# Performance work log

Measured on AMD Instinct MI355X. Metric: run time of the kernel, lower is better.

## Reference

```python
import jax, jax.numpy as jnp
import numpy as np

B, H, P, D, NF = 16, 16, 128, 128, 12  # patches == head_dim required by lin_qk


def setup_inputs() -> dict:
    key = jax.random.key(0)
    ks = jax.random.split(key, 8)
    return {
        "q": jax.random.normal(ks[0], (B, H, P, D), jnp.float32),
        "k": jax.random.normal(ks[1], (B, H, P, D), jnp.float32),
        "scale": jnp.ones((1,), jnp.float32),  # unused by the original forward
        "grid": jnp.arange(NF, dtype=jnp.float32) + 1.0,
        "base_weight": jax.random.uniform(ks[2], (D, D), jnp.float32),
        "coef_q": jax.random.uniform(ks[3], (D, NF), jnp.float32),
        "coef_k": jax.random.uniform(ks[4], (D, NF), jnp.float32),
        "scale_base": jnp.ones((1, H, P, D), jnp.float32),
        "scale_sp": jnp.ones((1, H, P, D), jnp.float32),
        "w_qk": jax.random.normal(ks[5], (D, D), jnp.float32) / np.float32(np.sqrt(D)),
        "b_qk": jnp.zeros((D,), jnp.float32),
    }


def _branch(x, coef, grid, base_weight, scale_sp, scale_base):
    # base path: SiLU(x) @ W^T  (F.linear semantics)
    base = jax.nn.silu(x) @ base_weight.T
    # KAN sin basis: sin(grid_f * x_d) -> (B,H,P,NF,D); contract coef[d,f]
    s = jnp.sin(grid[:, None] * x[..., None, :])
    f = jnp.einsum('df,bhpfd->bhpd', coef, s)
    return jax.nn.sigmoid(f * scale_sp + base * scale_base)


def reference(q, k, scale, grid, base_weight, coef_q, coef_k, scale_base, scale_sp, w_qk, b_qk):
    # Per-channel sigmoids, then sum over D. The original builds the full
    # (B,H,P,P,D) broadcast tensor sig_q[...,p,None,:] + sig_k[...,None,p',:]
    # and sums over D; that is exactly separable:
    #   sum_d(sig_q[p,d]) + sum_d(sig_k[p',d])
    sq = _branch(q, coef_q, grid, base_weight, scale_sp, scale_base).sum(-1)  # (B,H,P)
    sk = _branch(k, coef_k, grid, base_weight, scale_sp, scale_base).sum(-1)  # (B,H,P)
    f_out = sq[..., :, None] + sk[..., None, :]  # (B,H,P,P)
    f_out = f_out @ w_qk.T + b_qk  # lin_qk: valid because patches == head_dim
    return jax.nn.softmax(f_out, axis=-1)
```

## Files before the change

kernel.cpp:

```cpp
#include <hip/hip_runtime.h>
#include <hip/hip_bf16.h>


typedef float          f32x4 __attribute__((ext_vector_type(4)));
typedef short          s16x8 __attribute__((ext_vector_type(8)));
typedef unsigned short u16x8 __attribute__((ext_vector_type(8)));

static __device__ __forceinline__ unsigned short f2bf(float f) {
    __hip_bfloat16 h = __float2bfloat16(f);
    unsigned short r;
    __builtin_memcpy(&r, &h, 2);
    return r;
}
static __device__ __forceinline__ float fastrcp(float x) {
    return __builtin_amdgcn_rcpf(x);
}
static __device__ __forceinline__ int swz(int local) {
    return local ^ (((local >> 8) & 7) << 4);
}

__global__ __launch_bounds__(512, 4) void k_branch(
    const float* __restrict__ q, const float* __restrict__ k,
    const float* __restrict__ bw,
    const float* __restrict__ gridv,
    const float* __restrict__ coef_q, const float* __restrict__ coef_k,
    const float* __restrict__ sbase,
    const float* __restrict__ ssp,
    float* __restrict__ sums_lo, float* __restrict__ sums_hi)
{
    __shared__ char smem[32768];
    float* F_l = (float*)smem;

    const int t = threadIdx.x;
    const int lane = t & 63, w = t >> 6;
    const int wr = w >> 1;
    const int ch = w & 1;
    const int r15 = lane & 15, g4 = lane >> 4;
    const int row0 = blockIdx.x * 64;
    const bool is_q = row0 < 32768;
    const float* X = is_q ? q : k;
    const float* coef = is_q ? coef_q : coef_k;
    const int xrow0 = is_q ? row0 : row0 - 32768;
    const float g1 = gridv[0];

    #pragma unroll
    for (int it = 0; it < 4; ++it) {
        int c = it * 512 + t;
        const float4* wp = (const float4*)&bw[(c >> 4) * 128 + (c & 15) * 8];
        float4 w0 = wp[0], w1 = wp[1];
        float wv[8] = {w0.x, w0.y, w0.z, w0.w, w1.x, w1.y, w1.z, w1.w};
        u16x8 v;
        #pragma unroll
        for (int j = 0; j < 8; ++j) v[j] = f2bf(wv[j]);
        *(u16x8*)(smem + swz(c * 16)) = v;
    }
    __syncthreads();

    const float* xrowp = &X[(xrow0 + wr * 16 + r15) * 128];

    f32x4 acc[4];
    #pragma unroll
    for (int n = 0; n < 4; ++n) acc[n] = (f32x4){0.f, 0.f, 0.f, 0.f};

    #pragma unroll
    for (int s = 0; s < 4; ++s) {
        const float4* xp = (const float4*)&xrowp[s * 32 + g4 * 8];
        float4 x0 = xp[0], x1 = xp[1];
        float xsv[8] = {x0.x, x0.y, x0.z, x0.w, x1.x, x1.y, x1.z, x1.w};
        s16x8 af;
        #pragma unroll
        for (int j = 0; j < 8; ++j) {
            float s1 = xsv[j] * fastrcp(1.f + __expf(-xsv[j]));
            af[j] = (short)f2bf(s1);
        }
        #pragma unroll
        for (int n = 0; n < 4; ++n) {
            s16x8 bf = *(const s16x8*)(smem + swz((ch * 64 + n * 16 + r15) * 256
                                                  + s * 64 + g4 * 16));
            acc[n] = __builtin_amdgcn_mfma_f32_16x16x32_bf16(af, bf, acc[n], 0, 0, 0);
        }
    }
    __syncthreads();

    #pragma unroll
    for (int n = 0; n < 4; ++n) {
        int cl = n * 16 + r15;
        #pragma unroll
        for (int reg = 0; reg < 4; ++reg) {
            int rl = g4 * 4 + reg;
            F_l[(wr * 16 + rl) * 128 + ch * 64 + ((cl + rl * 4) & 63)] = acc[n][reg];
        }
    }

    const int ce = lane & 15;
    const int re = lane >> 4;
    float cf[4][12];
    #pragma unroll
    for (int j = 0; j < 4; ++j) {
        const float4* cp = (const float4*)&coef[(ch * 64 + ce * 4 + j) * 12];
        float4 c0 = cp[0], c1 = cp[1], c2 = cp[2];
        cf[j][0] = c0.x; cf[j][1] = c0.y; cf[j][2]  = c0.z; cf[j][3]  = c0.w;
        cf[j][4] = c1.x; cf[j][5] = c1.y; cf[j][6]  = c1.z; cf[j][7]  = c1.w;
        cf[j][8] = c2.x; cf[j][9] = c2.y; cf[j][10] = c2.z; cf[j][11] = c2.w;
    }

    #pragma unroll
    for (int i = 0; i < 4; ++i) {
        int rl = re * 4 + i;
        int rb = wr * 16 + rl;
        int grow = row0 + rb;
        int hp = grow & 2047;
        int gcol = ch * 64 + ce * 4;
        f32x4 F4 = *(f32x4*)&F_l[rb * 128 + ch * 64 + ((ce * 4 + rl * 4) & 63)];
        float4 x4 = *(const float4*)&X[(xrow0 + rb) * 128 + gcol];
        float4 sp = *(const float4*)&ssp[hp * 128 + gcol];
        float4 sb = *(const float4*)&sbase[hp * 128 + gcol];
        float xv[4]  = {x4.x, x4.y, x4.z, x4.w};
        float spv[4] = {sp.x, sp.y, sp.z, sp.w};
        float sbv[4] = {sb.x, sb.y, sb.z, sb.w};
        float ps = 0.f;
        #pragma unroll
        for (int j = 0; j < 4; ++j) {
            float a = g1 * xv[j];
            float s1 = __sinf(a);
            float cv = __cosf(a);
            float t2 = cv + cv;
            float sprev = 0.f, scur = s1;
            float f = cf[j][0] * s1;
            #pragma unroll
            for (int u = 1; u < 12; ++u) {
                float sn = __builtin_fmaf(t2, scur, -sprev);
                f = __builtin_fmaf(cf[j][u], sn, f);
                sprev = scur; scur = sn;
            }
            float z = f * spv[j] + F4[j] * sbv[j];
            ps += fastrcp(1.f + __expf(-z));
        }
        ps += __shfl_xor(ps, 1, 64);
        ps += __shfl_xor(ps, 2, 64);
        ps += __shfl_xor(ps, 4, 64);
        ps += __shfl_xor(ps, 8, 64);
        if (ce == 0) (ch ? sums_hi : sums_lo)[grow] = ps;
    }
}

__global__ __launch_bounds__(256) void k_attn(
    const float* __restrict__ sums_lo, const float* __restrict__ sums_hi,
    const float* __restrict__ w_qk, const float* __restrict__ b_qk,
    float* __restrict__ out)
{
    __shared__ float skl[128], Tl[128], Rl[128];
    const int bh = blockIdx.x >> 2;
    const int chunk = blockIdx.x & 3;
    const int t = threadIdx.x;

    if (t < 128) {
        int idx = 32768 + bh * 128 + t;
        skl[t] = sums_lo[idx] + sums_hi[idx];
    }
    __syncthreads();
    if (t < 128) {
        const float4* wr = (const float4*)&w_qk[t * 128];
        float a = 0.f, r = 0.f;
        #pragma unroll 8
        for (int p4 = 0; p4 < 32; ++p4) {
            float4 w4 = wr[p4];
            a += w4.x * skl[p4 * 4 + 0] + w4.y * skl[p4 * 4 + 1] +
                 w4.z * skl[p4 * 4 + 2] + w4.w * skl[p4 * 4 + 3];
            r += w4.x + w4.y + w4.z + w4.w;
        }
        Tl[t] = a + b_qk[t];
        Rl[t] = r;
    }
    __syncthreads();

    const int lane = t & 63, w = t >> 6;
    #pragma unroll
    for (int it = 0; it < 8; ++it) {
        int row = bh * 128 + chunk * 32 + it * 4 + w;
        float sqv = sums_lo[row] + sums_hi[row];
        float2 r2 = *(const float2*)&Rl[lane * 2];
        float2 t2 = *(const float2*)&Tl[lane * 2];
        float l0 = __builtin_fmaf(sqv, r2.x, t2.x);
        float l1 = __builtin_fmaf(sqv, r2.y, t2.y);
        float m = fmaxf(l0, l1);
        #pragma unroll
        for (int s = 32; s >= 1; s >>= 1) m = fmaxf(m, __shfl_xor(m, s, 64));
        float e0 = __expf(l0 - m), e1 = __expf(l1 - m);
        float sum = e0 + e1;
        #pragma unroll
        for (int w2 = 32; w2 >= 1; w2 >>= 1) sum += __shfl_xor(sum, w2, 64);
        float inv = __builtin_amdgcn_rcpf(sum);
        float2 o2 = {e0 * inv, e1 * inv};
        *(float2*)&out[row * 128 + lane * 2] = o2;
    }
}

extern "C" void kernel_launch(void* const* d_in, const int* in_sizes, int n_in,
                              void* d_out, int out_size, void* d_ws, size_t ws_size,
                              hipStream_t stream) {
    (void)in_sizes; (void)n_in; (void)out_size; (void)ws_size;
    const float* q      = (const float*)d_in[0];
    const float* k      = (const float*)d_in[1];
    const float* gridv  = (const float*)d_in[3];
    const float* bw     = (const float*)d_in[4];
    const float* coef_q = (const float*)d_in[5];
    const float* coef_k = (const float*)d_in[6];
    const float* sbase  = (const float*)d_in[7];
    const float* ssp    = (const float*)d_in[8];
    const float* w_qk   = (const float*)d_in[9];
    const float* b_qk   = (const float*)d_in[10];

    float* out  = (float*)d_out;
    float* ws      = (float*)d_ws;
    float* sums_lo = ws;
    float* sums_hi = ws + 65536;

    k_branch<<<1024, 512, 0, stream>>>(q, k, bw, gridv, coef_q, coef_k,
                                       sbase, ssp, sums_lo, sums_hi);
    k_attn<<<1024, 256, 0, stream>>>(sums_lo, sums_hi, w_qk, b_qk, out);
}
```

Baseline: 45.37 us.

## Use raw hardware exp/sin/bf16-pack instructions and halve attention grid

Replaces the library exp, sin/cos and bf16 conversions with inline v_exp_f32, v_fract+v_sin_f32 (revolution-scaled) and v_cvt_pk_bf16_f32 instructions, which cuts the range reduction and per-element conversion overhead. The attention kernel now runs 512 blocks, each covering 64 rows instead of 32, so the per-block w_qk matvec prologue is done half as often. The trade-off is less range and accuracy checking in the transcendentals, and fewer blocks available for parallelism in the second kernel.

```diff
diff --git a/kernel.cpp b/kernel.cpp
--- a/kernel.cpp
+++ b/kernel.cpp
@@ -4,16 +4,34 @@
 
 typedef float          f32x4 __attribute__((ext_vector_type(4)));
 typedef short          s16x8 __attribute__((ext_vector_type(8)));
-typedef unsigned short u16x8 __attribute__((ext_vector_type(8)));
-
-static __device__ __forceinline__ unsigned short f2bf(float f) {
-    __hip_bfloat16 h = __float2bfloat16(f);
-    unsigned short r;
-    __builtin_memcpy(&r, &h, 2);
+typedef int            s32x4 __attribute__((ext_vector_type(4)));
+typedef unsigned int   u32x4 __attribute__((ext_vector_type(4)));
+
+#define LOG2E   1.44269504f
+#define NLOG2E -1.44269504f
+#define INV2PI  0.15915494309189535f
+
+static __device__ __forceinline__ float hw_exp2(float x) {
+    float r;
+    asm("v_exp_f32 %0, %1" : "=v"(r) : "v"(x));
+    return r;
+}
+static __device__ __forceinline__ float hw_sin_rev(float rev) {
+    float f, r;
+    asm("v_fract_f32 %0, %1" : "=v"(f) : "v"(rev));
+    asm("v_sin_f32 %0, %1" : "=v"(r) : "v"(f));
     return r;
 }
 static __device__ __forceinline__ float fastrcp(float x) {
     return __builtin_amdgcn_rcpf(x);
+}
+static __device__ __forceinline__ unsigned int cvt_pk_bf16(float lo, float hi) {
+    unsigned int r;
+    asm("v_cvt_pk_bf16_f32 %0, %1, %2" : "=v"(r) : "v"(lo), "v"(hi));
+    return r;
+}
+static __device__ __forceinline__ float sigmoid_fast(float z) {
+    return fastrcp(1.f + hw_exp2(z * NLOG2E));
 }
 static __device__ __forceinline__ int swz(int local) {
     return local ^ (((local >> 8) & 7) << 4);
@@ -48,11 +66,9 @@
         int c = it * 512 + t;
         const float4* wp = (const float4*)&bw[(c >> 4) * 128 + (c & 15) * 8];
         float4 w0 = wp[0], w1 = wp[1];
-        float wv[8] = {w0.x, w0.y, w0.z, w0.w, w1.x, w1.y, w1.z, w1.w};
-        u16x8 v;
-        #pragma unroll
-        for (int j = 0; j < 8; ++j) v[j] = f2bf(wv[j]);
-        *(u16x8*)(smem + swz(c * 16)) = v;
+        u32x4 v = {cvt_pk_bf16(w0.x, w0.y), cvt_pk_bf16(w0.z, w0.w),
+                   cvt_pk_bf16(w1.x, w1.y), cvt_pk_bf16(w1.z, w1.w)};
+        *(u32x4*)(smem + swz(c * 16)) = v;
     }
     __syncthreads();
 
@@ -67,12 +83,15 @@
         const float4* xp = (const float4*)&xrowp[s * 32 + g4 * 8];
         float4 x0 = xp[0], x1 = xp[1];
         float xsv[8] = {x0.x, x0.y, x0.z, x0.w, x1.x, x1.y, x1.z, x1.w};
-        s16x8 af;
+        float sl[8];
         #pragma unroll
         for (int j = 0; j < 8; ++j) {
-            float s1 = xsv[j] * fastrcp(1.f + __expf(-xsv[j]));
-            af[j] = (short)f2bf(s1);
-        }
+            float e = hw_exp2(xsv[j] * NLOG2E);
+            sl[j] = xsv[j] * fastrcp(1.f + e);
+        }
+        s32x4 a4 = {(int)cvt_pk_bf16(sl[0], sl[1]), (int)cvt_pk_bf16(sl[2], sl[3]),
+                    (int)cvt_pk_bf16(sl[4], sl[5]), (int)cvt_pk_bf16(sl[6], sl[7])};
+        s16x8 af = __builtin_bit_cast(s16x8, a4);
         #pragma unroll
         for (int n = 0; n < 4; ++n) {
             s16x8 bf = *(const s16x8*)(smem + swz((ch * 64 + n * 16 + r15) * 256
@@ -104,6 +123,7 @@
         cf[j][8] = c2.x; cf[j][9] = c2.y; cf[j][10] = c2.z; cf[j][11] = c2.w;
     }
 
+    const float grev = g1 * INV2PI;
     #pragma unroll
     for (int i = 0; i < 4; ++i) {
         int rl = re * 4 + i;
@@ -121,9 +141,9 @@
         float ps = 0.f;
         #pragma unroll
         for (int j = 0; j < 4; ++j) {
-            float a = g1 * xv[j];
-            float s1 = __sinf(a);
-            float cv = __cosf(a);
+            float rev = grev * xv[j];
+            float s1 = hw_sin_rev(rev);
+            float cv = hw_sin_rev(rev + 0.25f);
             float t2 = cv + cv;
             float sprev = 0.f, scur = s1;
             float f = cf[j][0] * s1;
@@ -134,7 +154,7 @@
                 sprev = scur; scur = sn;
             }
             float z = f * spv[j] + F4[j] * sbv[j];
-            ps += fastrcp(1.f + __expf(-z));
+            ps += sigmoid_fast(z);
         }
         ps += __shfl_xor(ps, 1, 64);
         ps += __shfl_xor(ps, 2, 64);
@@ -150,8 +170,8 @@
     float* __restrict__ out)
 {
     __shared__ float skl[128], Tl[128], Rl[128];
-    const int bh = blockIdx.x >> 2;
-    const int chunk = blockIdx.x & 3;
+    const int bh = blockIdx.x >> 1;
+    const int half = blockIdx.x & 1;
     const int t = threadIdx.x;
 
     if (t < 128) {
@@ -176,8 +196,8 @@
 
     const int lane = t & 63, w = t >> 6;
     #pragma unroll
-    for (int it = 0; it < 8; ++it) {
-        int row = bh * 128 + chunk * 32 + it * 4 + w;
+    for (int it = 0; it < 16; ++it) {
+        int row = bh * 128 + half * 64 + it * 4 + w;
         float sqv = sums_lo[row] + sums_hi[row];
         float2 r2 = *(const float2*)&Rl[lane * 2];
         float2 t2 = *(const float2*)&Tl[lane * 2];
@@ -186,11 +206,12 @@
         float m = fmaxf(l0, l1);
         #pragma unroll
         for (int s = 32; s >= 1; s >>= 1) m = fmaxf(m, __shfl_xor(m, s, 64));
-        float e0 = __expf(l0 - m), e1 = __expf(l1 - m);
+        float e0 = hw_exp2((l0 - m) * LOG2E);
+        float e1 = hw_exp2((l1 - m) * LOG2E);
         float sum = e0 + e1;
         #pragma unroll
         for (int w2 = 32; w2 >= 1; w2 >>= 1) sum += __shfl_xor(sum, w2, 64);
-        float inv = __builtin_amdgcn_rcpf(sum);
+        float inv = fastrcp(sum);
         float2 o2 = {e0 * inv, e1 * inv};
         *(float2*)&out[row * 128 + lane * 2] = o2;
     }
@@ -218,5 +239,5 @@
 
     k_branch<<<1024, 512, 0, stream>>>(q, k, bw, gridv, coef_q, coef_k,
                                        sbase, ssp, sums_lo, sums_hi);
-    k_attn<<<1024, 256, 0, stream>>>(sums_lo, sums_hi, w_qk, b_qk, out);
-}
+    k_attn<<<512, 256, 0, stream>>>(sums_lo, sums_hi, w_qk, b_qk, out);
+}
```

Measured after the change: 42.80 us. 1.06x faster.
